# Kernel optimization log

Measured on AMD Instinct MI355X. Metric: run time of the kernel, lower is better.

## Reference

```python
import jax, jax.numpy as jnp
import numpy as np

D = 64          # internal token dim (patch_encoder output)
E = 4           # num_experts
HID = 256       # expert hidden dim
NCLS = 10       # classifier output (hardcoded in source)


def gelu(x):
    return jax.nn.gelu(x, approximate=False)  # torch nn.GELU default = exact erf


def setup_inputs() -> dict:
    key = jax.random.key(0)
    ks = jax.random.split(key, 16)
    B, S, IN = 128, 1024, 192
    sc = lambda k, sh, fan: (jax.random.normal(k, sh, jnp.float32) / np.sqrt(fan))
    return {
        "x": jax.random.normal(ks[0], (B, S, IN), jnp.float32),
        # patch encoder: Linear(IN,64) -> GELU -> Linear(64,D)
        "pe_w1": sc(ks[1], (IN, 64), IN), "pe_b1": jnp.zeros((64,), jnp.float32),
        "pe_w2": sc(ks[2], (64, D), 64),  "pe_b2": jnp.zeros((D,), jnp.float32),
        # gate: Linear(D, E)
        "gate_w": sc(ks[3], (D, E), D), "gate_b": jnp.zeros((E,), jnp.float32),
        # experts: per-expert MLP D -> HID -> D
        "ew1": sc(ks[4], (E, D, HID), D), "eb1": jnp.zeros((E, HID), jnp.float32),
        "ew2": sc(ks[5], (E, HID, D), HID), "eb2": jnp.zeros((E, D), jnp.float32),
        # classifier: LayerNorm(D) -> Linear(D,D) -> GELU -> Linear(D,10)
        "ln_g": jnp.ones((D,), jnp.float32), "ln_b": jnp.zeros((D,), jnp.float32),
        "cl_w1": sc(ks[6], (D, D), D), "cl_b1": jnp.zeros((D,), jnp.float32),
        "cl_w2": sc(ks[7], (D, NCLS), D), "cl_b2": jnp.zeros((NCLS,), jnp.float32),
    }


def reference(x, pe_w1, pe_b1, pe_w2, pe_b2, gate_w, gate_b,
              ew1, eb1, ew2, eb2, ln_g, ln_b, cl_w1, cl_b1, cl_w2, cl_b2):
    # patch encoder: [B,S,IN] -> [B,S,D]
    h = gelu(x @ pe_w1 + pe_b1) @ pe_w2 + pe_b2

    # top-1 gating
    gate_logits = h @ gate_w + gate_b                      # [B,S,E]
    probs = jax.nn.softmax(gate_logits, axis=-1)
    top1 = jnp.argmax(probs, axis=-1)                      # [B,S] int
    onehot = jax.nn.one_hot(top1, E, dtype=h.dtype)        # [B,S,E] dispatch mask
    gate = jnp.sum(probs * onehot, axis=-1)                # [B,S] top-1 gate value

    # expert MLPs computed densely, combined by one-hot mask (same math as dispatch)
    eh = gelu(jnp.einsum('bsd,edh->bseh', h, ew1) + eb1)   # [B,S,E,HID]
    eo = jnp.einsum('bseh,ehd->bsed', eh, ew2) + eb2       # [B,S,E,D]
    moe_out = jnp.einsum('bsed,bse->bsd', eo, onehot) * gate[..., None]

    # switch-style load-balance aux loss: E * sum_e f_e * P_e
    f = jnp.mean(onehot, axis=(0, 1))                      # fraction routed per expert
    p = jnp.mean(probs, axis=(0, 1))                       # mean gate prob per expert
    aux_loss = E * jnp.sum(f * p)

    # mean pool over sequence, then classifier
    z = jnp.mean(moe_out, axis=1)                          # [B,D]
    mu = jnp.mean(z, axis=-1, keepdims=True)
    var = jnp.var(z, axis=-1, keepdims=True)
    zn = (z - mu) * jax.lax.rsqrt(var + 1e-5) * ln_g + ln_b
    y = gelu(zn @ cl_w1 + cl_b1) @ cl_w2 + cl_b2           # [B,10]
    return (y, aux_loss)
```

## Files before the change

kernel.cpp:

```cpp
#include <hip/hip_runtime.h>
#include <hip/hip_bf16.h>
#include <math.h>

typedef unsigned int  u32;
typedef unsigned short u16;
typedef unsigned long long u64;

using bf16x8  = __attribute__((ext_vector_type(8))) __bf16;
using float4v = __attribute__((ext_vector_type(4))) float;

#define MFMA16(a,b,c) __builtin_amdgcn_mfma_f32_16x16x32_bf16(a,b,c,0,0,0)

#define W1P_OFF   0u
#define W2P_OFF   24576u
#define GWP_OFF   40960u
#define E1P_OFF   43008u
#define E2P_OFF   174080u
#define ZF_OFF    305152u
#define CNTF_OFF  337920u
#define PSUMF_OFF 337984u
#define FAST_WS_BYTES 338048u

#define Z_OFF    0u
#define CNT_OFF  32768u
#define PSUM_OFF 32832u

__device__ inline u16 f2bf(float f){
  union { float f; u32 u; } v; v.f = f;
  u32 r = v.u + 0x7fffu + ((v.u >> 16) & 1u);
  return (u16)(r >> 16);
}
__device__ inline u32 pk2(float a, float b){
  union { __hip_bfloat162 h2; u32 u; } v;
  v.h2 = __float22bfloat162_rn(make_float2(a, b));
  return v.u;
}

__device__ inline float geluf(float x){
  float u = fabsf(x) * 0.70710678118654752f;
  float t = __builtin_amdgcn_rcpf(1.0f + 0.3275911f * u);
  float poly = t*(0.254829592f + t*(-0.284496736f +
               t*(1.421413741f + t*(-1.453152027f + t*1.061405429f))));
  float er = 1.0f - poly * __expf(-u*u);
  return 0.5f * x * (1.0f + copysignf(er, x));
}

__global__ __launch_bounds__(256) void k0_pack(
    const float* __restrict__ w1, const float* __restrict__ w2, const float* __restrict__ gw,
    const float* __restrict__ e1, const float* __restrict__ e2,
    u16* w1p, u16* w2p, u16* gwp, u16* e1p, u16* e2p,
    float* z, u32* cnt, float* psum)
{
  int p = blockIdx.x*256 + threadIdx.x;
  if (p < 12288){
    int k = p >> 6, m = p & 63;
    int kc = k>>5, q = (k>>3)&3, j = k&7, mt = m>>4, col = m&15;
    w1p[((kc*4+mt)*64 + q*16+col)*8 + j] = f2bf(w1[p]); return;
  }
  p -= 12288;
  if (p < 4096){
    int k = p >> 6, m = p & 63;
    int kc = k>>5, q = (k>>3)&3, j = k&7, mt = m>>4, col = m&15;
    w2p[((kc*4+mt)*64 + q*16+col)*8 + j] = f2bf(w2[p]); return;
  }
  p -= 4096;
  if (p < 1024){
    int j = p & 7, lane = (p>>3) & 63;
    int col = lane & 15, q = lane >> 4, kc = p >> 9;
    int k = kc*32 + q*8 + j;
    gwp[p] = (col < 4) ? f2bf(gw[k*4 + col]) : (u16)0; return;
  }
  p -= 1024;
  if (p < 65536){
    int e = p >> 14, r = p & 16383;
    int k = r >> 8, m = r & 255;
    int kc = k>>5, q = (k>>3)&3, j = k&7, mt = m>>4, col = m&15;
    e1p[e*16384 + ((kc*16+mt)*64 + q*16+col)*8 + j] = f2bf(e1[p]); return;
  }
  p -= 65536;
  if (p < 65536){
    int e = p >> 14, r = p & 16383;
    int k = r >> 6, m = r & 63;
    int kc = k>>5, q = (k>>3)&3, j = k&7, mt = m>>4, col = m&15;
    e2p[e*16384 + ((kc*4+mt)*64 + q*16+col)*8 + j] = f2bf(e2[p]); return;
  }
  p -= 65536;
  if (p < 8192){ z[p] = 0.f; return; }
  p -= 8192;
  if (p < 4){ cnt[p] = 0u; return; }
  p -= 4;
  if (p < 4){ psum[p] = 0.f; return; }
}

__global__ __launch_bounds__(256) void kMain(
    const float* __restrict__ x,
    const float* __restrict__ b1, const float* __restrict__ b2, const float* __restrict__ gb,
    const u16* __restrict__ w1p, const u16* __restrict__ w2p, const u16* __restrict__ gwp,
    const u16* __restrict__ e1p, const u16* __restrict__ e2p,
    const float* __restrict__ eb1, const float* __restrict__ eb2,
    float* __restrict__ z, u32* __restrict__ cnt, float* __restrict__ psum)
{
  __shared__ char wreg[25600];
  __shared__ char hl[9216];
  __shared__ int   be_s[64];
  __shared__ float gv_s[64];
  __shared__ int   sperm[64];
  __shared__ int   se_s[64];
  __shared__ float sg_s[64];
  __shared__ float lgp[4];
  __shared__ u32   lgc[4];

  const int tid  = threadIdx.x;
  const int lane = tid & 63, wave = tid >> 6;
  const int col  = lane & 15, quad = lane >> 4;
  const int tok0 = blockIdx.x * 64;
  const int t    = wave*16 + col;
  if (tid < 4){ lgp[tid] = 0.f; lgc[tid] = 0u; }

  char* wr = wreg + wave*6400;

  const float* xw = x + (size_t)(tok0 + wave*16)*192;
  for (int it = 0; it < 6; ++it){
    int task = it*64 + lane;
    int tr = task / 24, c = task % 24;
    float4 f0 = *(const float4*)(xw + tr*192 + c*8);
    float4 f1 = *(const float4*)(xw + tr*192 + c*8 + 4);
    uint4 v;
    v.x = pk2(f0.x,f0.y); v.y = pk2(f0.z,f0.w);
    v.z = pk2(f1.x,f1.y); v.w = pk2(f1.z,f1.w);
    *(uint4*)(wr + tr*400 + c*16) = v;
  }

  bf16x8 bx[6];
  for (int kc = 0; kc < 6; ++kc)
    bx[kc] = *(const bf16x8*)(wr + col*400 + (4*kc+quad)*16);

  char* h1t = wr;
  for (int mt = 0; mt < 4; ++mt){
    float4v acc = {0.f,0.f,0.f,0.f};
    for (int kc = 0; kc < 6; ++kc){
      bf16x8 a = *(const bf16x8*)(w1p + ((kc*4 + mt)*64 + lane)*8);
      acc = MFMA16(a, bx[kc], acc);
    }
    int j0 = mt*16 + quad*4;
    float4 bb = *(const float4*)(b1 + j0);
    uint2 w; w.x = pk2(geluf(acc[0]+bb.x), geluf(acc[1]+bb.y));
             w.y = pk2(geluf(acc[2]+bb.z), geluf(acc[3]+bb.w));
    *(uint2*)(h1t + col*144 + mt*32 + quad*8) = w;
  }

  {
    bf16x8 bh1[2];
    for (int kc = 0; kc < 2; ++kc)
      bh1[kc] = *(const bf16x8*)(h1t + col*144 + (4*kc+quad)*16);
    for (int mt = 0; mt < 4; ++mt){
      float4v acc = {0.f,0.f,0.f,0.f};
      for (int kc = 0; kc < 2; ++kc){
        bf16x8 a = *(const bf16x8*)(w2p + ((kc*4 + mt)*64 + lane)*8);
        acc = MFMA16(a, bh1[kc], acc);
      }
      int j0 = mt*16 + quad*4;
      float4 bb = *(const float4*)(b2 + j0);
      uint2 w; w.x = pk2(acc[0]+bb.x, acc[1]+bb.y);
               w.y = pk2(acc[2]+bb.z, acc[3]+bb.w);
      *(uint2*)(hl + t*144 + mt*32 + quad*8) = w;
    }
  }

  float p0=0.f,p1=0.f,p2=0.f,p3=0.f; int be=0;
  {
    bf16x8 bh[2];
    for (int kc = 0; kc < 2; ++kc)
      bh[kc] = *(const bf16x8*)(hl + t*144 + (4*kc+quad)*16);
    float4v ag = {0.f,0.f,0.f,0.f};
    for (int kc = 0; kc < 2; ++kc){
      bf16x8 a = *(const bf16x8*)(gwp + (kc*64 + lane)*8);
      ag = MFMA16(a, bh[kc], ag);
    }
    if (quad == 0){
      float l0 = ag[0]+gb[0], l1 = ag[1]+gb[1], l2 = ag[2]+gb[2], l3 = ag[3]+gb[3];
      float mx = fmaxf(fmaxf(l0,l1), fmaxf(l2,l3));
      float x0 = __expf(l0-mx), x1 = __expf(l1-mx), x2 = __expf(l2-mx), x3 = __expf(l3-mx);
      float inv = __builtin_amdgcn_rcpf(x0+x1+x2+x3);
      p0 = x0*inv; p1 = x1*inv; p2 = x2*inv; p3 = x3*inv;
      float bv = l0; be = 0;
      if (l1 > bv){ bv = l1; be = 1; }
      if (l2 > bv){ bv = l2; be = 2; }
      if (l3 > bv){ bv = l3; be = 3; }
      be_s[t] = be;
      gv_s[t] = (be==0) ? p0 : (be==1) ? p1 : (be==2) ? p2 : p3;
    }
  }
  __syncthreads();
  if (quad == 0){
    atomicAdd(&lgp[0], p0); atomicAdd(&lgp[1], p1);
    atomicAdd(&lgp[2], p2); atomicAdd(&lgp[3], p3);
    atomicAdd(&lgc[be], 1u);
  }

  if (tid < 64){
    int e = be_s[tid];
    u64 m0 = __ballot(e==0), m1 = __ballot(e==1), m2 = __ballot(e==2), m3 = __ballot(e==3);
    int c0 = __popcll(m0), c1 = __popcll(m1), c2 = __popcll(m2);
    int base = (e==0) ? 0 : (e==1) ? c0 : (e==2) ? c0+c1 : c0+c1+c2;
    u64 me = (e==0) ? m0 : (e==1) ? m1 : (e==2) ? m2 : m3;
    int pos = base + __popcll(me & ((1ull<<tid)-1ull));
    sperm[pos] = tid; se_s[pos] = e; sg_s[pos] = gv_s[tid];
  }
  __syncthreads();

  const int slice = wave*16;
  const int tt    = sperm[slice + col];
  const int myE   = se_s[slice + col];
  const float myG = sg_s[slice + col];
  const int e_lo  = se_s[slice], e_hi = se_s[slice + 15];
  char* hbt = wr;

  bf16x8 bhp[2];
  for (int kc = 0; kc < 2; ++kc)
    bhp[kc] = *(const bf16x8*)(hl + tt*144 + (4*kc+quad)*16);

  float oacc[16];
  for (int i = 0; i < 16; ++i) oacc[i] = 0.f;

  for (int e = e_lo; e <= e_hi; ++e){
    const u16* W1 = e1p + e*16384;
    const u16* W2 = e2p + e*16384;
    float4v accE[4];
    for (int mt = 0; mt < 4; ++mt) accE[mt] = (float4v){0.f,0.f,0.f,0.f};
    for (int p = 0; p < 4; ++p){
      for (int mt2 = 0; mt2 < 4; ++mt2){
        float4v acc = {0.f,0.f,0.f,0.f};
        for (int kc = 0; kc < 2; ++kc){
          bf16x8 a = *(const bf16x8*)(W1 + ((kc*16 + p*4 + mt2)*64 + lane)*8);
          acc = MFMA16(a, bhp[kc], acc);
        }
        int j0 = p*64 + mt2*16 + quad*4;
        float4 bb = *(const float4*)(eb1 + e*256 + j0);
        uint2 w; w.x = pk2(geluf(acc[0]+bb.x), geluf(acc[1]+bb.y));
                 w.y = pk2(geluf(acc[2]+bb.z), geluf(acc[3]+bb.w));
        *(uint2*)(hbt + col*144 + mt2*32 + quad*8) = w;
      }
      bf16x8 bq0 = *(const bf16x8*)(hbt + col*144 + quad*16);
      bf16x8 bq1 = *(const bf16x8*)(hbt + col*144 + (4+quad)*16);
      for (int mt = 0; mt < 4; ++mt){
        bf16x8 a0 = *(const bf16x8*)(W2 + (((p*2+0)*4 + mt)*64 + lane)*8);
        bf16x8 a1 = *(const bf16x8*)(W2 + (((p*2+1)*4 + mt)*64 + lane)*8);
        accE[mt] = MFMA16(a0, bq0, accE[mt]);
        accE[mt] = MFMA16(a1, bq1, accE[mt]);
      }
    }
    float wgt = (myE == e) ? myG : 0.f;
    for (int mt = 0; mt < 4; ++mt){
      float4 bb = *(const float4*)(eb2 + e*64 + mt*16 + quad*4);
      oacc[mt*4+0] += (accE[mt][0] + bb.x) * wgt;
      oacc[mt*4+1] += (accE[mt][1] + bb.y) * wgt;
      oacc[mt*4+2] += (accE[mt][2] + bb.z) * wgt;
      oacc[mt*4+3] += (accE[mt][3] + bb.w) * wgt;
    }
  }

  for (int m = 1; m < 16; m <<= 1)
    for (int i = 0; i < 16; ++i)
      oacc[i] += __shfl_xor(oacc[i], m, 64);
  if (col == 0){
    float* pw = (float*)wr;
    for (int mt = 0; mt < 4; ++mt)
      for (int r = 0; r < 4; ++r)
        pw[mt*16 + quad*4 + r] = oacc[mt*4 + r];
  }
  __syncthreads();
  int b = blockIdx.x >> 4;
  if (tid < 64){
    float s = *(const float*)(wreg + tid*4)         + *(const float*)(wreg + 6400 + tid*4)
            + *(const float*)(wreg + 12800 + tid*4) + *(const float*)(wreg + 19200 + tid*4);
    atomicAdd(&z[b*64 + tid], s);
  }
  if (tid < 4){ atomicAdd(&cnt[tid], lgc[tid]); atomicAdd(&psum[tid], lgp[tid]); }
}

__global__ __launch_bounds__(64) void kFinal(
    const float* __restrict__ z, const u32* __restrict__ cnt, const float* __restrict__ psum,
    const float* __restrict__ ln_g, const float* __restrict__ ln_b,
    const float* __restrict__ cw1, const float* __restrict__ cb1,
    const float* __restrict__ cw2, const float* __restrict__ cb2,
    float* __restrict__ out)
{
  __shared__ float z_l[64], zn_l[64], c1_l[64], red[2];
  int tid = threadIdx.x, b = blockIdx.x;
  z_l[tid] = z[b*64 + tid] * (1.0f/1024.0f);
  __syncthreads();
  if (tid == 0){
    float mu = 0.f; for (int i=0;i<64;++i) mu += z_l[i]; mu *= (1.f/64.f);
    float vv = 0.f; for (int i=0;i<64;++i){ float d=z_l[i]-mu; vv += d*d; } vv *= (1.f/64.f);
    red[0]=mu; red[1]=1.0f/sqrtf(vv+1e-5f);
  }
  __syncthreads();
  zn_l[tid] = (z_l[tid]-red[0])*red[1]*ln_g[tid] + ln_b[tid];
  __syncthreads();
  float a1 = cb1[tid];
  for (int k=0;k<64;++k) a1 += zn_l[k]*cw1[k*64+tid];
  c1_l[tid] = geluf(a1);
  __syncthreads();
  if (tid < 10){
    float y = cb2[tid];
    for (int k=0;k<64;++k) y += c1_l[k]*cw2[k*10+tid];
    out[b*10+tid] = y;
  }
  if (b == 0 && tid == 0){
    float aux = 0.f;
    for (int e=0;e<4;++e) aux += (float)cnt[e]*psum[e];
    out[1280] = 4.0f*aux/(131072.0f*131072.0f);
  }
}

__global__ __launch_bounds__(256) void kInitF(float* z, u32* cnt, float* psum){
  int i = blockIdx.x*256 + threadIdx.x;
  if (i < 8192) z[i] = 0.f;
  if (i < 4){ cnt[i] = 0u; psum[i] = 0.f; }
}

__global__ __launch_bounds__(256) void kFusedF(
    const float* __restrict__ x,
    const float* __restrict__ w1, const float* __restrict__ b1,
    const float* __restrict__ w2, const float* __restrict__ b2,
    const float* __restrict__ gw, const float* __restrict__ gb,
    const float* __restrict__ e1, const float* __restrict__ eb1,
    const float* __restrict__ e2, const float* __restrict__ eb2,
    float* __restrict__ z, u32* __restrict__ cnt, float* __restrict__ psum)
{
  __shared__ float xs[4][192];
  __shared__ float h1s[4][64];
  __shared__ float hs[4][64];
  __shared__ float hid[4][256];
  __shared__ float lg[4][4];
  __shared__ int   be_s[4];
  __shared__ float gv_s[4];
  __shared__ float lgp[4];
  __shared__ u32   lgc[4];
  const int tid  = threadIdx.x;
  const int w    = tid >> 6, lane = tid & 63;
  const int tok  = blockIdx.x*4 + w;
  if (tid < 4){ lgp[tid] = 0.f; lgc[tid] = 0u; }
  for (int r = 0; r < 3; ++r)
    xs[w][lane + 64*r] = x[(size_t)tok*192 + lane + 64*r];
  __syncthreads();
  float a = b1[lane];
  for (int k = 0; k < 192; ++k) a += xs[w][k]*w1[k*64 + lane];
  h1s[w][lane] = geluf(a);
  __syncthreads();
  float h = b2[lane];
  for (int k = 0; k < 64; ++k) h += h1s[w][k]*w2[k*64 + lane];
  hs[w][lane] = h;
  __syncthreads();
  if (lane < 4){
    float l = gb[lane];
    for (int k = 0; k < 64; ++k) l += hs[w][k]*gw[k*4 + lane];
    lg[w][lane] = l;
  }
  __syncthreads();
  if (lane == 0){
    float l0=lg[w][0], l1=lg[w][1], l2=lg[w][2], l3=lg[w][3];
    float mx = fmaxf(fmaxf(l0,l1),fmaxf(l2,l3));
    float x0=expf(l0-mx), x1=expf(l1-mx), x2=expf(l2-mx), x3=expf(l3-mx);
    float inv = 1.f/(x0+x1+x2+x3);
    float p0=x0*inv, p1=x1*inv, p2=x2*inv, p3=x3*inv;
    int be=0; float bv=l0;
    if (l1>bv){bv=l1;be=1;}
    if (l2>bv){bv=l2;be=2;}
    if (l3>bv){bv=l3;be=3;}
    be_s[w]=be;
    gv_s[w]=(be==0)?p0:(be==1)?p1:(be==2)?p2:p3;
    atomicAdd(&lgp[0],p0); atomicAdd(&lgp[1],p1);
    atomicAdd(&lgp[2],p2); atomicAdd(&lgp[3],p3);
    atomicAdd(&lgc[be],1u);
  }
  __syncthreads();
  const int e    = be_s[w];
  const float gv = gv_s[w];
  const float* W1 = e1 + e*16384;
  const float* W2 = e2 + e*16384;
  for (int q = 0; q < 4; ++q){
    int j = q*64 + lane;
    float s = eb1[e*256 + j];
    for (int k = 0; k < 64; ++k) s += hs[w][k]*W1[k*256 + j];
    hid[w][j] = geluf(s);
  }
  __syncthreads();
  float o = eb2[e*64 + lane];
  for (int j = 0; j < 256; ++j) o += hid[w][j]*W2[j*64 + lane];
  int b = tok >> 10;
  atomicAdd(&z[b*64 + lane], o*gv);
  __syncthreads();
  if (tid < 4){ atomicAdd(&cnt[tid], lgc[tid]); atomicAdd(&psum[tid], lgp[tid]); }
}

extern "C" void kernel_launch(void* const* d_in, const int* in_sizes, int n_in,
                              void* d_out, int out_size, void* d_ws, size_t ws_size,
                              hipStream_t stream)
{
  const float* x    = (const float*)d_in[0];
  const float* pw1  = (const float*)d_in[1];
  const float* pb1  = (const float*)d_in[2];
  const float* pw2  = (const float*)d_in[3];
  const float* pb2  = (const float*)d_in[4];
  const float* gw   = (const float*)d_in[5];
  const float* gb   = (const float*)d_in[6];
  const float* ew1  = (const float*)d_in[7];
  const float* eb1  = (const float*)d_in[8];
  const float* ew2  = (const float*)d_in[9];
  const float* eb2  = (const float*)d_in[10];
  const float* lng  = (const float*)d_in[11];
  const float* lnb  = (const float*)d_in[12];
  const float* cw1  = (const float*)d_in[13];
  const float* cb1  = (const float*)d_in[14];
  const float* cw2  = (const float*)d_in[15];
  const float* cb2  = (const float*)d_in[16];
  char* ws  = (char*)d_ws;
  float* out = (float*)d_out;

  if (ws_size >= FAST_WS_BYTES){
    u16*  w1p  = (u16*)(ws + W1P_OFF);
    u16*  w2p  = (u16*)(ws + W2P_OFF);
    u16*  gwp  = (u16*)(ws + GWP_OFF);
    u16*  e1p  = (u16*)(ws + E1P_OFF);
    u16*  e2p  = (u16*)(ws + E2P_OFF);
    float* z    = (float*)(ws + ZF_OFF);
    u32*  cnt  = (u32*)(ws + CNTF_OFF);
    float* psum = (float*)(ws + PSUMF_OFF);
    k0_pack<<<613, 256, 0, stream>>>(pw1, pw2, gw, ew1, ew2,
                                     w1p, w2p, gwp, e1p, e2p, z, cnt, psum);
    kMain <<<2048, 256, 0, stream>>>(x, pb1, pb2, gb, w1p, w2p, gwp, e1p, e2p,
                                     eb1, eb2, z, cnt, psum);
    kFinal<<<128, 64, 0, stream>>>(z, cnt, psum, lng, lnb, cw1, cb1, cw2, cb2, out);
  } else {
    float* z    = (float*)(ws + Z_OFF);
    u32*   cnt  = (u32*)(ws + CNT_OFF);
    float* psum = (float*)(ws + PSUM_OFF);
    kInitF <<<32,    256, 0, stream>>>(z, cnt, psum);
    kFusedF<<<32768, 256, 0, stream>>>(x, pw1, pb1, pw2, pb2, gw, gb,
                                       ew1, eb1, ew2, eb2, z, cnt, psum);
    kFinal <<<128,   64,  0, stream>>>(z, cnt, psum, lng, lnb, cw1, cb1, cw2, cb2, out);
  }
}
```

Baseline: 271.0 us.

## Halve per-wave LDS staging of x and vectorize weight packing writes

The x tile is now staged into LDS in two halves of 96 columns, which halves the per-wave staging buffer and the total shared memory per block. The aim is to fit more blocks per CU and raise occupancy for the main kernel. The pack kernel now has each thread gather eight strided fp32 weights and write one 16-byte bf16 vector, cutting its grid from 613 to 105 blocks. The trade-off is an extra staging round per wave and strided, uncoalesced reads in the pack kernel.

```diff
diff --git a/kernel.cpp b/kernel.cpp
--- a/kernel.cpp
+++ b/kernel.cpp
@@ -51,45 +51,73 @@
     u16* w1p, u16* w2p, u16* gwp, u16* e1p, u16* e2p,
     float* z, u32* cnt, float* psum)
 {
-  int p = blockIdx.x*256 + threadIdx.x;
-  if (p < 12288){
-    int k = p >> 6, m = p & 63;
-    int kc = k>>5, q = (k>>3)&3, j = k&7, mt = m>>4, col = m&15;
-    w1p[((kc*4+mt)*64 + q*16+col)*8 + j] = f2bf(w1[p]); return;
-  }
-  p -= 12288;
-  if (p < 4096){
-    int k = p >> 6, m = p & 63;
-    int kc = k>>5, q = (k>>3)&3, j = k&7, mt = m>>4, col = m&15;
-    w2p[((kc*4+mt)*64 + q*16+col)*8 + j] = f2bf(w2[p]); return;
-  }
-  p -= 4096;
-  if (p < 1024){
-    int j = p & 7, lane = (p>>3) & 63;
-    int col = lane & 15, q = lane >> 4, kc = p >> 9;
-    int k = kc*32 + q*8 + j;
-    gwp[p] = (col < 4) ? f2bf(gw[k*4 + col]) : (u16)0; return;
-  }
-  p -= 1024;
-  if (p < 65536){
-    int e = p >> 14, r = p & 16383;
-    int k = r >> 8, m = r & 255;
-    int kc = k>>5, q = (k>>3)&3, j = k&7, mt = m>>4, col = m&15;
-    e1p[e*16384 + ((kc*16+mt)*64 + q*16+col)*8 + j] = f2bf(e1[p]); return;
-  }
-  p -= 65536;
-  if (p < 65536){
-    int e = p >> 14, r = p & 16383;
-    int k = r >> 6, m = r & 63;
-    int kc = k>>5, q = (k>>3)&3, j = k&7, mt = m>>4, col = m&15;
-    e2p[e*16384 + ((kc*4+mt)*64 + q*16+col)*8 + j] = f2bf(e2[p]); return;
-  }
-  p -= 65536;
-  if (p < 8192){ z[p] = 0.f; return; }
-  p -= 8192;
-  if (p < 4){ cnt[p] = 0u; return; }
-  p -= 4;
-  if (p < 4){ psum[p] = 0.f; return; }
+  int d = blockIdx.x*256 + threadIdx.x;
+  int lane = d & 63, col = lane & 15, q = lane >> 4;
+  if (d < 1536){
+    int tile = d >> 6, kc = tile >> 2, mt = tile & 3;
+    int m = mt*16 + col, k0 = kc*32 + q*8;
+    uint4 v;
+    v.x = pk2(w1[(k0+0)*64+m], w1[(k0+1)*64+m]);
+    v.y = pk2(w1[(k0+2)*64+m], w1[(k0+3)*64+m]);
+    v.z = pk2(w1[(k0+4)*64+m], w1[(k0+5)*64+m]);
+    v.w = pk2(w1[(k0+6)*64+m], w1[(k0+7)*64+m]);
+    *(uint4*)(w1p + d*8) = v; return;
+  }
+  d -= 1536;
+  if (d < 512){
+    int tile = d >> 6, kc = tile >> 2, mt = tile & 3;
+    int m = mt*16 + col, k0 = kc*32 + q*8;
+    uint4 v;
+    v.x = pk2(w2[(k0+0)*64+m], w2[(k0+1)*64+m]);
+    v.y = pk2(w2[(k0+2)*64+m], w2[(k0+3)*64+m]);
+    v.z = pk2(w2[(k0+4)*64+m], w2[(k0+5)*64+m]);
+    v.w = pk2(w2[(k0+6)*64+m], w2[(k0+7)*64+m]);
+    *(uint4*)(w2p + d*8) = v; return;
+  }
+  d -= 512;
+  if (d < 128){
+    int kc = d >> 6, k0 = kc*32 + q*8;
+    uint4 v = {0u,0u,0u,0u};
+    if (col < 4){
+      v.x = pk2(gw[(k0+0)*4+col], gw[(k0+1)*4+col]);
+      v.y = pk2(gw[(k0+2)*4+col], gw[(k0+3)*4+col]);
+      v.z = pk2(gw[(k0+4)*4+col], gw[(k0+5)*4+col]);
+      v.w = pk2(gw[(k0+6)*4+col], gw[(k0+7)*4+col]);
+    }
+    *(uint4*)(gwp + d*8) = v; return;
+  }
+  d -= 128;
+  if (d < 8192){
+    int e = d >> 11, t2 = d & 2047;
+    int tile = t2 >> 6, kc = tile >> 4, mt = tile & 15;
+    int m = mt*16 + col, k0 = kc*32 + q*8;
+    const float* s = e1 + e*16384;
+    uint4 v;
+    v.x = pk2(s[(k0+0)*256+m], s[(k0+1)*256+m]);
+    v.y = pk2(s[(k0+2)*256+m], s[(k0+3)*256+m]);
+    v.z = pk2(s[(k0+4)*256+m], s[(k0+5)*256+m]);
+    v.w = pk2(s[(k0+6)*256+m], s[(k0+7)*256+m]);
+    *(uint4*)(e1p + d*8) = v; return;
+  }
+  d -= 8192;
+  if (d < 8192){
+    int e = d >> 11, t2 = d & 2047;
+    int tile = t2 >> 6, kc = tile >> 2, mt = tile & 3;
+    int m = mt*16 + col, k0 = kc*32 + q*8;
+    const float* s = e2 + e*16384;
+    uint4 v;
+    v.x = pk2(s[(k0+0)*64+m], s[(k0+1)*64+m]);
+    v.y = pk2(s[(k0+2)*64+m], s[(k0+3)*64+m]);
+    v.z = pk2(s[(k0+4)*64+m], s[(k0+5)*64+m]);
+    v.w = pk2(s[(k0+6)*64+m], s[(k0+7)*64+m]);
+    *(uint4*)(e2p + d*8) = v; return;
+  }
+  d -= 8192;
+  if (d < 8192){ z[d] = 0.f; return; }
+  d -= 8192;
+  if (d < 4){ cnt[d] = 0u; return; }
+  d -= 4;
+  if (d < 4){ psum[d] = 0.f; return; }
 }
 
 __global__ __launch_bounds__(256) void kMain(
@@ -100,7 +128,7 @@
     const float* __restrict__ eb1, const float* __restrict__ eb2,
     float* __restrict__ z, u32* __restrict__ cnt, float* __restrict__ psum)
 {
-  __shared__ char wreg[25600];
+  __shared__ char wreg[13312];
   __shared__ char hl[9216];
   __shared__ int   be_s[64];
   __shared__ float gv_s[64];
@@ -117,23 +145,25 @@
   const int t    = wave*16 + col;
   if (tid < 4){ lgp[tid] = 0.f; lgc[tid] = 0u; }
 
-  char* wr = wreg + wave*6400;
+  char* wr = wreg + wave*3328;
 
   const float* xw = x + (size_t)(tok0 + wave*16)*192;
-  for (int it = 0; it < 6; ++it){
-    int task = it*64 + lane;
-    int tr = task / 24, c = task % 24;
-    float4 f0 = *(const float4*)(xw + tr*192 + c*8);
-    float4 f1 = *(const float4*)(xw + tr*192 + c*8 + 4);
-    uint4 v;
-    v.x = pk2(f0.x,f0.y); v.y = pk2(f0.z,f0.w);
-    v.z = pk2(f1.x,f1.y); v.w = pk2(f1.z,f1.w);
-    *(uint4*)(wr + tr*400 + c*16) = v;
-  }
-
   bf16x8 bx[6];
-  for (int kc = 0; kc < 6; ++kc)
-    bx[kc] = *(const bf16x8*)(wr + col*400 + (4*kc+quad)*16);
+  for (int h = 0; h < 2; ++h){
+    for (int it = 0; it < 3; ++it){
+      int task = it*64 + lane;
+      int tr = task / 12, c = task % 12;
+      const float* src = xw + tr*192 + h*96 + c*8;
+      float4 f0 = *(const float4*)(src);
+      float4 f1 = *(const float4*)(src + 4);
+      uint4 v;
+      v.x = pk2(f0.x,f0.y); v.y = pk2(f0.z,f0.w);
+      v.z = pk2(f1.x,f1.y); v.w = pk2(f1.z,f1.w);
+      *(uint4*)(wr + tr*208 + c*16) = v;
+    }
+    for (int kc = 0; kc < 3; ++kc)
+      bx[h*3 + kc] = *(const bf16x8*)(wr + col*208 + (4*kc + quad)*16);
+  }
 
   char* h1t = wr;
   for (int mt = 0; mt < 4; ++mt){
@@ -272,8 +302,8 @@
   __syncthreads();
   int b = blockIdx.x >> 4;
   if (tid < 64){
-    float s = *(const float*)(wreg + tid*4)         + *(const float*)(wreg + 6400 + tid*4)
-            + *(const float*)(wreg + 12800 + tid*4) + *(const float*)(wreg + 19200 + tid*4);
+    float s = *(const float*)(wreg + tid*4)        + *(const float*)(wreg + 3328 + tid*4)
+            + *(const float*)(wreg + 6656 + tid*4) + *(const float*)(wreg + 9984 + tid*4);
     atomicAdd(&z[b*64 + tid], s);
   }
   if (tid < 4){ atomicAdd(&cnt[tid], lgc[tid]); atomicAdd(&psum[tid], lgp[tid]); }
@@ -428,7 +458,7 @@
     float* z    = (float*)(ws + ZF_OFF);
     u32*  cnt  = (u32*)(ws + CNTF_OFF);
     float* psum = (float*)(ws + PSUMF_OFF);
-    k0_pack<<<613, 256, 0, stream>>>(pw1, pw2, gw, ew1, ew2,
+    k0_pack<<<105, 256, 0, stream>>>(pw1, pw2, gw, ew1, ew2,
                                      w1p, w2p, gwp, e1p, e2p, z, cnt, psum);
     kMain <<<2048, 256, 0, stream>>>(x, pb1, pb2, gb, w1p, w2p, gwp, e1p, e2p,
                                      eb1, eb2, z, cnt, psum);
```

Result: slower. 278.4 us (+2.7%).
